# Kernel optimization log

Hardware: AMD Instinct MI355X
Metric: run time of the kernel (lower is better)

Reference implementation:

```python
import jax, jax.numpy as jnp
import numpy as np
from jax import lax

B, T, N, E, M = 2, 24, 1500, 2000, 4000
DIM, NLY, K = 64, 2, 3
H = DIM + DIM // 2  # 96: GAT input dim after concat with NodeEdge output


def setup_inputs():
    ks = iter(jax.random.split(jax.random.key(0), 100))
    def rn(shape, scale=1.0):
        return jax.random.normal(next(ks), shape, dtype=jnp.float32) * scale
    d = {}
    d["x_in"] = rn((B, T, N, 4)); d["e_in"] = rn((B, T, E, 3))
    d["b_in"] = rn((B, T, N, 4)); d["a_in"] = rn((B, T, E, 3))
    def lin(name, din, dout):
        d[name + "_W"] = rn((din, dout), 1.0 / float(np.sqrt(din)))
        d[name + "_b"] = jnp.zeros((dout,), jnp.float32)
    lin("enc0", 4, DIM); lin("enc1", 3, DIM)
    lin("enc2", 4, DIM // 2); lin("enc3", 3, DIM // 2)
    d["inci"] = jax.random.uniform(next(ks), (N, E), dtype=jnp.float32)
    for p in ("s1", "s2"):
        for g in ("gx", "ge"):
            d[p + "_" + g + "_W"] = rn((NLY, H, DIM), 0.1)
            d[p + "_" + g + "_as"] = rn((NLY, DIM), 0.1)
            d[p + "_" + g + "_ad"] = rn((NLY, DIM), 0.1)
            d[p + "_" + g + "_b"] = jnp.zeros((NLY, DIM), jnp.float32)
        d[p + "_ne_W"] = rn((NLY, DIM, DIM // 2), 0.125)
        d[p + "_ne_b"] = jnp.zeros((NLY, DIM // 2), jnp.float32)
        d[p + "_ne_w"] = rn((NLY, N, E), 0.02)
        d[p + "_ne_p"] = jnp.zeros((NLY, N, E), jnp.float32)
        d[p + "_en_W"] = rn((NLY, DIM, DIM // 2), 0.125)
        d[p + "_en_b"] = jnp.zeros((NLY, DIM // 2), jnp.float32)
        d[p + "_en_w"] = rn((NLY, E, N), 0.02)
        d[p + "_en_p"] = jnp.zeros((NLY, E, N), jnp.float32)
        d[p + "_tp_W"] = rn((NLY, DIM, DIM, K), 0.07)
        d[p + "_tp_b"] = jnp.zeros((NLY, DIM), jnp.float32)
    lin("conc", H, DIM); lin("res", DIM, DIM); lin("out", DIM, 1)
    d["edge_ind"] = jax.random.randint(next(ks), (2, E), 0, N)
    d["node_ind"] = jax.random.randint(next(ks), (2, M), 0, E)
    return d


def gat(x, src, dst, n, W, a_s, a_d, bias):
    # PyG GATConv (heads=1, concat=True, neg_slope=0.2); self-loops already in src/dst.
    # x: [B,T,n,din] -> G=B*T independent graphs (the batched edge_index replication
    # of BatchGATConv is exactly equivalent to vmapping over graph replicas).
    g = x.reshape(B * T, n, x.shape[-1])
    z = g @ W                                    # [G,n,DIM]
    es = jnp.einsum('gnd,d->gn', z, a_s)
    ed = jnp.einsum('gnd,d->gn', z, a_d)
    alpha = jax.nn.leaky_relu(es[:, src] + ed[:, dst], 0.2)   # [G,Etot]
    def one(a, zz):
        m = jax.ops.segment_max(a, dst, num_segments=n)
        ex = jnp.exp(a - m[dst])
        s = jax.ops.segment_sum(ex, dst, num_segments=n)
        w = ex / s[dst]
        return jax.ops.segment_sum(w[:, None] * zz[src], dst, num_segments=n)
    out = jax.vmap(one)(alpha, z) + bias
    return out.reshape(B, T, n, DIM)


def node_edge(inp, W, b, w, p, A):
    # NodeEdge: relu(Linear(dim->dim//2)) then incidence-masked matmul
    xe = jax.nn.relu(inp @ W + b)                # [B,T,*,DIM//2]
    return jnp.einsum('ne,btef->btnf', w * A + p, xe)


def causal_conv(h, W, b, dil):
    # h: [M,C,T]; left-pad (K-1)*dil -> causal dilated Conv1d
    pad = (K - 1) * dil
    out = lax.conv_general_dilated(h, W, (1,), [(pad, 0)], rhs_dilation=(dil,),
                                   dimension_numbers=('NCH', 'OIH', 'NCH'))
    return out + b[None, :, None]


def stblock(x, e, src_n, dst_n, src_e, dst_e, inc, P):
    (gxW, gxas, gxad, gxb, geW, geas, gead, geb,
     neW, neb, new, nep, enW, enb, enw, enp, tpW, tpb) = P
    incT = inc.T
    for l in range(NLY):
        xe = node_edge(e, neW[l], neb[l], new[l], nep[l], inc)
        x = jax.nn.relu(gat(jnp.concatenate([x, xe], -1), src_n, dst_n, N,
                            gxW[l], gxas[l], gxad[l], gxb[l]))
        ex = node_edge(x, enW[l], enb[l], enw[l], enp[l], incT)
        e = jax.nn.relu(gat(jnp.concatenate([e, ex], -1), src_e, dst_e, E,
                            geW[l], geas[l], gead[l], geb[l]))
    xt = x.transpose(0, 2, 3, 1).reshape(B * N, DIM, T)   # 'b t n d -> (b n) d t'
    et = e.transpose(0, 2, 3, 1).reshape(B * E, DIM, T)
    h = jnp.concatenate([xt, et], axis=0)
    for l in range(NLY):
        h = jax.nn.relu(causal_conv(h, tpW[l], tpb[l], 2 ** l))
    x = h[:B * N].reshape(B, N, DIM, T).transpose(0, 3, 1, 2)
    e = h[B * N:].reshape(B, E, DIM, T).transpose(0, 3, 1, 2)
    return x, e


def _forward(x_in, e_in, b_in, a_in, enc0_W, enc0_b, enc1_W, enc1_b, enc2_W, enc2_b,
             enc3_W, enc3_b, inci,
             s1_gx_W, s1_gx_as, s1_gx_ad, s1_gx_b, s1_ge_W, s1_ge_as, s1_ge_ad, s1_ge_b,
             s1_ne_W, s1_ne_b, s1_ne_w, s1_ne_p, s1_en_W, s1_en_b, s1_en_w, s1_en_p,
             s1_tp_W, s1_tp_b,
             s2_gx_W, s2_gx_as, s2_gx_ad, s2_gx_b, s2_ge_W, s2_ge_as, s2_ge_ad, s2_ge_b,
             s2_ne_W, s2_ne_b, s2_ne_w, s2_ne_p, s2_en_W, s2_en_b, s2_en_w, s2_en_p,
             s2_tp_W, s2_tp_b,
             conc_W, conc_b, res_W, res_b, out_W, out_b, edge_ind, node_ind):
    # add self-loops once (GATConv add_self_loops=True)
    src_n = jnp.concatenate([edge_ind[0], jnp.arange(N)])
    dst_n = jnp.concatenate([edge_ind[1], jnp.arange(N)])
    src_e = jnp.concatenate([node_ind[0], jnp.arange(E)])
    dst_e = jnp.concatenate([node_ind[1], jnp.arange(E)])
    inc = jnp.abs(inci)
    x = x_in @ enc0_W + enc0_b
    e = e_in @ enc1_W + enc1_b
    bb = jax.nn.relu(b_in @ enc2_W + enc2_b)
    aa = jax.nn.relu(a_in @ enc3_W + enc3_b)
    res_x = jnp.broadcast_to(x[:, -1:], (B, T, N, DIM))   # pre-relu last step, tiled
    res_e = jnp.broadcast_to(e[:, -1:], (B, T, E, DIM))
    x = jax.nn.relu(x); e = jax.nn.relu(e)
    P1 = (s1_gx_W, s1_gx_as, s1_gx_ad, s1_gx_b, s1_ge_W, s1_ge_as, s1_ge_ad, s1_ge_b,
          s1_ne_W, s1_ne_b, s1_ne_w, s1_ne_p, s1_en_W, s1_en_b, s1_en_w, s1_en_p,
          s1_tp_W, s1_tp_b)
    P2 = (s2_gx_W, s2_gx_as, s2_gx_ad, s2_gx_b, s2_ge_W, s2_ge_as, s2_ge_ad, s2_ge_b,
          s2_ne_W, s2_ne_b, s2_ne_w, s2_ne_p, s2_en_W, s2_en_b, s2_en_w, s2_en_p,
          s2_tp_W, s2_tp_b)
    x, e = stblock(x, e, src_n, dst_n, src_e, dst_e, inc, P1)
    # concs is [Linear]*2 in torch -> shared weights for both branches
    x = jax.nn.relu(jnp.concatenate([x, bb], -1) @ conc_W + conc_b)
    e = jax.nn.relu(jnp.concatenate([e, aa], -1) @ conc_W + conc_b)
    x, e = stblock(x, e, src_n, dst_n, src_e, dst_e, inc, P2)
    x = jax.nn.relu(jnp.cumsum(x @ res_W + res_b, axis=1) + res_x)
    e = jax.nn.relu(jnp.cumsum(e @ res_W + res_b, axis=1) + res_e)
    out = jnp.clip((x @ out_W + out_b) / 6.0 + 0.5, 0.0, 1.0)   # F.hardsigmoid
    eo = jnp.tanh(e @ out_W + out_b)
    return out, eo


def reference(x_in, e_in, b_in, a_in, enc0_W, enc0_b, enc1_W, enc1_b, enc2_W, enc2_b,
              enc3_W, enc3_b, inci,
              s1_gx_W, s1_gx_as, s1_gx_ad, s1_gx_b, s1_ge_W, s1_ge_as, s1_ge_ad, s1_ge_b,
              s1_ne_W, s1_ne_b, s1_ne_w, s1_ne_p, s1_en_W, s1_en_b, s1_en_w, s1_en_p,
              s1_tp_W, s1_tp_b,
              s2_gx_W, s2_gx_as, s2_gx_ad, s2_gx_b, s2_ge_W, s2_ge_as, s2_ge_ad, s2_ge_b,
              s2_ne_W, s2_ne_b, s2_ne_w, s2_ne_p, s2_en_W, s2_en_b, s2_en_w, s2_en_p,
              s2_tp_W, s2_tp_b,
              conc_W, conc_b, res_W, res_b, out_W, out_b, edge_ind, node_ind):
    return _forward(x_in, e_in, b_in, a_in, enc0_W, enc0_b, enc1_W, enc1_b, enc2_W,
                    enc2_b, enc3_W, enc3_b, inci,
                    s1_gx_W, s1_gx_as, s1_gx_ad, s1_gx_b, s1_ge_W, s1_ge_as, s1_ge_ad,
                    s1_ge_b, s1_ne_W, s1_ne_b, s1_ne_w, s1_ne_p, s1_en_W, s1_en_b,
                    s1_en_w, s1_en_p, s1_tp_W, s1_tp_b,
                    s2_gx_W, s2_gx_as, s2_gx_ad, s2_gx_b, s2_ge_W, s2_ge_as, s2_ge_ad,
                    s2_ge_b, s2_ne_W, s2_ne_b, s2_ne_w, s2_ne_p, s2_en_W, s2_en_b,
                    s2_en_w, s2_en_p, s2_tp_W, s2_tp_b,
                    conc_W, conc_b, res_W, res_b, out_W, out_b, edge_ind, node_ind)
```

## Files before the change

### kernel.cpp

```cpp
#include <hip/hip_runtime.h>
#include <hip/hip_bf16.h>
#include <cfloat>
#include <math.h>

typedef __hip_bfloat16 bf16;
typedef __attribute__((ext_vector_type(8))) short short8v;
typedef __attribute__((ext_vector_type(4))) float f32x4;

constexpr int B_ = 2, T_ = 24, N_ = 1500, E_ = 2000, M_ = 4000, G_ = 48;
constexpr int KPN = 2048;
constexpr int KPE = 1536;

__device__ __forceinline__ float b2f(bf16 v) { return __bfloat162float(v); }
__device__ __forceinline__ bf16 f2b(float v) { return __float2bfloat16(v); }
static inline int ceilDiv(int a, int b) { return (a + b - 1) / b; }

__global__ __launch_bounds__(256) void k_sentinel(float* __restrict__ out, int n, float val) {
  int i = blockIdx.x * 256 + threadIdx.x;
  if (i < n) out[i] = val;
}

__device__ __forceinline__ void wprep_body(int i, const float* g0, const float* e0, const float* g1,
                                           const float* e1, const float* cw, const float* rw,
                                           const float* t0, const float* t1, bf16* out) {
  if (i >= 108544) return;
  float v;
  if (i < 49152) {
    int which = i / 12288, r = i % 12288;
    const float* W = which == 0 ? g0 : which == 1 ? e0 : which == 2 ? g1 : e1;
    int l = r / 6144, j = r % 6144;
    int n = j / 96, k = j % 96;
    v = W[l * 6144 + k * 64 + n];
  } else if (i < 55296) {
    int j = i - 49152, n = j / 96, k = j % 96;
    v = cw[k * 64 + n];
  } else if (i < 59392) {
    int j = i - 55296, n = j / 64, k = j % 64;
    v = rw[k * 64 + n];
  } else {
    int r = i - 59392;
    int which = r / 24576;
    const float* W = which ? t1 : t0;
    int rr = r % 24576;
    int l = rr / 12288, j = rr % 12288;
    int ii = j & 63, o = (j >> 6) & 63, k = j >> 12;
    v = W[l * 12288 + o * 192 + ii * 3 + k];
  }
  out[i] = f2b(v);
}

__device__ __forceinline__ void enc_body(int idx, int din, const float* in, const float* W,
                                         const float* bias, bf16* out, float* last, int nodes) {
  if (idx >= G_ * nodes * 64) return;
  int d = idx & 63;
  int row = idx >> 6;
  int node = row % nodes;
  int g = row / nodes;
  const float* ir = in + (size_t)row * din;
  float acc = bias[d];
  for (int i = 0; i < din; i++) acc += ir[i] * W[i * 64 + d];
  if (g % T_ == T_ - 1) last[((size_t)(g / T_) * nodes + node) * 64 + d] = acc;
  out[idx] = f2b(fmaxf(acc, 0.f));
}

constexpr int NB_W = (108544 + 255) / 256;
constexpr int NB_EX = G_ * N_ * 64 / 256;
constexpr int NB_EE = G_ * E_ * 64 / 256;
__global__ __launch_bounds__(256) void k_begin(const float* __restrict__ g0, const float* __restrict__ e0,
                                               const float* __restrict__ g1, const float* __restrict__ e1,
                                               const float* __restrict__ cw, const float* __restrict__ rw,
                                               const float* __restrict__ t0, const float* __restrict__ t1,
                                               bf16* __restrict__ wAll,
                                               const float* __restrict__ x_in, const float* __restrict__ encxW,
                                               const float* __restrict__ encxB, bf16* __restrict__ xbuf,
                                               float* __restrict__ lastx,
                                               const float* __restrict__ e_in, const float* __restrict__ enceW,
                                               const float* __restrict__ enceB, bf16* __restrict__ ebuf,
                                               float* __restrict__ laste) {
  int bid = blockIdx.x, tid = threadIdx.x;
  if (bid < NB_W) {
    wprep_body(bid * 256 + tid, g0, e0, g1, e1, cw, rw, t0, t1, wAll);
  } else if (bid < NB_W + NB_EX) {
    enc_body((bid - NB_W) * 256 + tid, 4, x_in, encxW, encxB, xbuf, lastx, N_);
  } else {
    enc_body((bid - NB_W - NB_EX) * 256 + tid, 3, e_in, enceW, enceB, ebuf, laste, E_);
  }
}

template <int DIN, int DOUT>
__global__ __launch_bounds__(256) void k_enc2(const float* __restrict__ in, const float* __restrict__ W,
                                              const float* __restrict__ bias, bf16* __restrict__ out,
                                              int nodes) {
  int idx = blockIdx.x * 256 + threadIdx.x;
  if (idx >= G_ * nodes * DOUT) return;
  int d = idx % DOUT;
  int row = idx / DOUT;
  const float* ir = in + (size_t)row * DIN;
  float acc = bias[d];
#pragma unroll
  for (int i = 0; i < DIN; i++) acc += ir[i] * W[i * DOUT + d];
  out[idx] = f2b(fmaxf(acc, 0.f));
}

__device__ __forceinline__ void lin_neT_body(float* sh, int g, int n0, int t, const bf16* act,
                                             const float* W, const float* bias, bf16* outT,
                                             int nodes, int Kp) {
  float* As = sh;
  float* Ws = sh + 4160;
  float* bs = sh + 4160 + 2048;
  for (int i = t; i < 2048; i += 256) Ws[i] = W[i];
  if (t < 32) bs[t] = bias[t];
  {
    int r = t >> 2, ch = t & 3;
    int node = n0 + r;
    short tmp[16];
    if (node < nodes) {
      const bf16* src = act + ((size_t)g * nodes + node) * 64 + ch * 16;
      *reinterpret_cast<uint4*>(tmp) = *reinterpret_cast<const uint4*>(src);
      *reinterpret_cast<uint4*>(tmp + 8) = *reinterpret_cast<const uint4*>(src + 8);
#pragma unroll
      for (int j = 0; j < 16; j++) As[r * 65 + ch * 16 + j] = b2f(*reinterpret_cast<bf16*>(&tmp[j]));
    } else {
#pragma unroll
      for (int j = 0; j < 16; j++) As[r * 65 + ch * 16 + j] = 0.f;
    }
  }
  __syncthreads();
  int nd = t & 63, fq = t >> 6;
  float acc[8];
#pragma unroll
  for (int j = 0; j < 8; j++) acc[j] = bs[fq * 8 + j];
  for (int i = 0; i < 64; i++) {
    float a = As[nd * 65 + i];
#pragma unroll
    for (int j = 0; j < 8; j++) acc[j] += a * Ws[i * 32 + fq * 8 + j];
  }
  bool valid = (n0 + nd) < nodes;
#pragma unroll
  for (int j = 0; j < 8; j++) {
    float v = valid ? fmaxf(acc[j], 0.f) : 0.f;
    outT[(size_t)(g * 32 + fq * 8 + j) * Kp + n0 + nd] = f2b(v);
  }
}

constexpr int NBL_N = (KPN / 64) * G_;
constexpr int NBM_N = (N_ * KPN + 255) / 256;
__global__ __launch_bounds__(256) void k_prepN(const bf16* __restrict__ act, const float* __restrict__ W,
                                               const float* __restrict__ bias, bf16* __restrict__ outT,
                                               const float* __restrict__ w, const float* __restrict__ p,
                                               const float* __restrict__ inci, bf16* __restrict__ mat) {
  __shared__ float sh[4160 + 2048 + 32];
  int bid = blockIdx.x, tid = threadIdx.x;
  if (bid < NBL_N) {
    lin_neT_body(sh, bid / (KPN / 64), (bid % (KPN / 64)) * 64, tid, act, W, bias, outT, E_, KPN);
  } else {
    int i = (bid - NBL_N) * 256 + tid;
    if (i < N_ * KPN) {
      int row = i / KPN, k = i % KPN;
      float v = 0.f;
      if (k < E_) {
        size_t o = (size_t)row * E_ + k;
        v = w[o] * fabsf(inci[o]) + p[o];
      }
      mat[i] = f2b(v);
    }
  }
}

constexpr int NBL_E = (KPE / 64) * G_;
constexpr int NBT_E = 63 * (KPE / 32);
__global__ __launch_bounds__(256) void k_prepE(const bf16* __restrict__ act, const float* __restrict__ W,
                                               const float* __restrict__ bias, bf16* __restrict__ outT,
                                               const float* __restrict__ w, const float* __restrict__ p,
                                               const float* __restrict__ inci, bf16* __restrict__ mat) {
  __shared__ float sh[4160 + 2048 + 32];
  int bid = blockIdx.x, tid = threadIdx.x;
  if (bid < NBL_E) {
    lin_neT_body(sh, bid / (KPE / 64), (bid % (KPE / 64)) * 64, tid, act, W, bias, outT, N_, KPE);
  } else {
    float* tl = sh;
    int mt = bid - NBL_E;
    int e0 = (mt % 63) * 32, n0 = (mt / 63) * 32;
    int tx = tid & 31, ty = tid >> 5;
    for (int r = ty; r < 32; r += 8) {
      int n = n0 + r, e = e0 + tx;
      tl[r * 33 + tx] = (n < N_ && e < E_) ? fabsf(inci[(size_t)n * E_ + e]) : 0.f;
    }
    __syncthreads();
    for (int r = ty; r < 32; r += 8) {
      int e = e0 + r, n = n0 + tx;
      if (e < E_ && n < KPE) {
        size_t o = (size_t)e * N_ + n;
        mat[(size_t)e * KPE + n] = (n < N_) ? f2b(tl[tx * 33 + r] * w[o] + p[o]) : f2b(0.f);
      }
    }
  }
}

__global__ __launch_bounds__(256) void k_mgemm64(const bf16* __restrict__ A0, const bf16* __restrict__ Bt,
                                                 bf16* __restrict__ Cp, int Mm, int Kp, int Nn, int gy) {
  __shared__ __align__(16) short As[4][4][64][8];
  __shared__ __align__(16) short Bs[4][4][128][8];
  int tid = threadIdx.x;
  int nwg = gridDim.x;
  int bid = blockIdx.x;
  int l = (bid & 7) * (nwg >> 3) + (bid >> 3);
  int bm = (l % gy) * 64, bn = (l / gy) * 128;
  int lane = tid & 63, wid = tid >> 6;
  int wr = wid >> 1, wc = wid & 1;
  f32x4 acc[2][4];
#pragma unroll
  for (int i = 0; i < 2; i++)
#pragma unroll
    for (int j = 0; j < 4; j++) acc[i][j] = f32x4{0.f, 0.f, 0.f, 0.f};

  const int sr = tid >> 2;
  const int sc = tid & 3;
  const int br = tid >> 1;
  const int bh = tid & 1;
  const int kb = lane >> 4, lr = lane & 15;
  const int gmA = bm + sr;
  const bool va_ok = (gmA < Mm);
  const bf16* ap = A0 + (size_t)gmA * Kp + sc * 8;
  const bf16* bp = Bt + (size_t)(bn + br) * Kp + bh * 16;
  const uint4 z4 = {0, 0, 0, 0};
  const int P = Kp >> 5;

  uint4 va0 = va_ok ? *reinterpret_cast<const uint4*>(ap) : z4;
  uint4 vb0a = *reinterpret_cast<const uint4*>(bp);
  uint4 vb0b = *reinterpret_cast<const uint4*>(bp + 8);
  uint4 va1 = va_ok ? *reinterpret_cast<const uint4*>(ap + 32) : z4;
  uint4 vb1a = *reinterpret_cast<const uint4*>(bp + 32);
  uint4 vb1b = *reinterpret_cast<const uint4*>(bp + 40);
  *reinterpret_cast<uint4*>(&As[0][sc][sr][0]) = va0;
  *reinterpret_cast<uint4*>(&Bs[0][bh * 2 + 0][br][0]) = vb0a;
  *reinterpret_cast<uint4*>(&Bs[0][bh * 2 + 1][br][0]) = vb0b;
  uint4 va2 = va_ok ? *reinterpret_cast<const uint4*>(ap + 64) : z4;
  uint4 vb2a = *reinterpret_cast<const uint4*>(bp + 64);
  uint4 vb2b = *reinterpret_cast<const uint4*>(bp + 72);
  __syncthreads();

  for (int p = 0; p < P; p += 2) {
    *reinterpret_cast<uint4*>(&As[(p + 1) & 3][sc][sr][0]) = va1;
    *reinterpret_cast<uint4*>(&Bs[(p + 1) & 3][bh * 2 + 0][br][0]) = vb1a;
    *reinterpret_cast<uint4*>(&Bs[(p + 1) & 3][bh * 2 + 1][br][0]) = vb1b;
    if (p + 3 < P) {
      va1 = va_ok ? *reinterpret_cast<const uint4*>(ap + (p + 3) * 32) : z4;
      vb1a = *reinterpret_cast<const uint4*>(bp + (p + 3) * 32);
      vb1b = *reinterpret_cast<const uint4*>(bp + (p + 3) * 32 + 8);
    }
    {
      int bf = p & 3;
      short8v a0 = *reinterpret_cast<const short8v*>(&As[bf][kb][wr * 32 + lr][0]);
      short8v a1 = *reinterpret_cast<const short8v*>(&As[bf][kb][wr * 32 + 16 + lr][0]);
      short8v b[4];
#pragma unroll
      for (int ni = 0; ni < 4; ni++)
        b[ni] = *reinterpret_cast<const short8v*>(&Bs[bf][kb][wc * 64 + ni * 16 + lr][0]);
      __builtin_amdgcn_s_setprio(1);
#pragma unroll
      for (int ni = 0; ni < 4; ni++) {
        acc[0][ni] = __builtin_amdgcn_mfma_f32_16x16x32_bf16(a0, b[ni], acc[0][ni], 0, 0, 0);
        acc[1][ni] = __builtin_amdgcn_mfma_f32_16x16x32_bf16(a1, b[ni], acc[1][ni], 0, 0, 0);
      }
      __builtin_amdgcn_s_setprio(0);
    }
    __syncthreads();
    *reinterpret_cast<uint4*>(&As[(p + 2) & 3][sc][sr][0]) = va2;
    *reinterpret_cast<uint4*>(&Bs[(p + 2) & 3][bh * 2 + 0][br][0]) = vb2a;
    *reinterpret_cast<uint4*>(&Bs[(p + 2) & 3][bh * 2 + 1][br][0]) = vb2b;
    if (p + 4 < P) {
      va2 = va_ok ? *reinterpret_cast<const uint4*>(ap + (p + 4) * 32) : z4;
      vb2a = *reinterpret_cast<const uint4*>(bp + (p + 4) * 32);
      vb2b = *reinterpret_cast<const uint4*>(bp + (p + 4) * 32 + 8);
    }
    {
      int bf = (p + 1) & 3;
      short8v a0 = *reinterpret_cast<const short8v*>(&As[bf][kb][wr * 32 + lr][0]);
      short8v a1 = *reinterpret_cast<const short8v*>(&As[bf][kb][wr * 32 + 16 + lr][0]);
      short8v b[4];
#pragma unroll
      for (int ni = 0; ni < 4; ni++)
        b[ni] = *reinterpret_cast<const short8v*>(&Bs[bf][kb][wc * 64 + ni * 16 + lr][0]);
      __builtin_amdgcn_s_setprio(1);
#pragma unroll
      for (int ni = 0; ni < 4; ni++) {
        acc[0][ni] = __builtin_amdgcn_mfma_f32_16x16x32_bf16(a0, b[ni], acc[0][ni], 0, 0, 0);
        acc[1][ni] = __builtin_amdgcn_mfma_f32_16x16x32_bf16(a1, b[ni], acc[1][ni], 0, 0, 0);
      }
      __builtin_amdgcn_s_setprio(0);
    }
    __syncthreads();
  }
#pragma unroll
  for (int mi = 0; mi < 2; mi++) {
    int r0 = bm + wr * 32 + mi * 16 + (lane >> 4) * 4;
#pragma unroll
    for (int ni = 0; ni < 4; ni++) {
      int col = bn + wc * 64 + ni * 16 + lr;
#pragma unroll
      for (int i = 0; i < 4; i++) {
        int r = r0 + i;
        if (r < Mm) Cp[(size_t)r * Nn + col] = f2b(acc[mi][ni][i]);
      }
    }
  }
}

template <int AMODE, int KOCT, bool CF32b, bool ESED>
__global__ __launch_bounds__(256) void k_mgemm96(const bf16* __restrict__ A0, const bf16* __restrict__ A1,
                                                 const bf16* __restrict__ Bt, void* __restrict__ Cp,
                                                 int Mm, int nodes,
                                                 const float* __restrict__ bias, int relu,
                                                 const float* __restrict__ asv, const float* __restrict__ adv,
                                                 float* __restrict__ esOut, float* __restrict__ edOut) {
  constexpr int KP = KOCT * 8;
  __shared__ __align__(16) short As[KOCT][128][8];
  __shared__ __align__(16) short Bs[KOCT][64][8];
  __shared__ float smr[2][128][2];
  int tid = threadIdx.x;
  int bm = blockIdx.y * 128;
  int lane = tid & 63, wid = tid >> 6;
  int wr = wid >> 1, wc = wid & 1;
  const int kb = lane >> 4, lr = lane & 15;
  const uint4 z4 = {0, 0, 0, 0};

  {
    int ar = tid >> 1, ah = tid & 1;
    int gm = bm + ar;
    bool ok = (gm < Mm);
    int gdiv = 0, gmod = 0;
    if (AMODE == 1 && ok) { gdiv = gm / nodes; gmod = gm % nodes; }
#pragma unroll
    for (int c = 0; c < KOCT / 4; c++) {
      int ks = c * 32 + ah * 16;
      uint4 va0 = z4, va1 = z4;
      if (ok) {
        const bf16* src;
        if (AMODE == 0) src = A0 + (size_t)gm * KP + ks;
        else if (ks < 64) src = A0 + (size_t)gm * 64 + ks;
        else if (AMODE == 1) src = A1 + ((size_t)gmod * G_ + gdiv) * 32 + (ks - 64);
        else src = A1 + (size_t)gm * 32 + (ks - 64);
        const uint4* p = reinterpret_cast<const uint4*>(src);
        va0 = p[0];
        va1 = p[1];
      }
      *reinterpret_cast<uint4*>(&As[c * 4 + ah * 2 + 0][ar][0]) = va0;
      *reinterpret_cast<uint4*>(&As[c * 4 + ah * 2 + 1][ar][0]) = va1;
    }
  }
  {
    int br = tid >> 2, bk = tid & 3;
#pragma unroll
    for (int c = 0; c < KOCT / 4; c++) {
      int o = c * 4 + bk;
      uint4 vb = *reinterpret_cast<const uint4*>(Bt + (size_t)br * KP + o * 8);
      *reinterpret_cast<uint4*>(&Bs[o][br][0]) = vb;
    }
  }
  __syncthreads();

  f32x4 acc[4][2];
#pragma unroll
  for (int i = 0; i < 4; i++)
#pragma unroll
    for (int j = 0; j < 2; j++) acc[i][j] = f32x4{0.f, 0.f, 0.f, 0.f};

#pragma unroll
  for (int c = 0; c < KOCT / 4; c++) {
    short8v a[4], b[2];
#pragma unroll
    for (int mi = 0; mi < 4; mi++)
      a[mi] = *reinterpret_cast<const short8v*>(&As[c * 4 + kb][wr * 64 + mi * 16 + lr][0]);
#pragma unroll
    for (int ni = 0; ni < 2; ni++)
      b[ni] = *reinterpret_cast<const short8v*>(&Bs[c * 4 + kb][wc * 32 + ni * 16 + lr][0]);
    __builtin_amdgcn_s_setprio(1);
#pragma unroll
    for (int mi = 0; mi < 4; mi++)
#pragma unroll
      for (int ni = 0; ni < 2; ni++)
        acc[mi][ni] = __builtin_amdgcn_mfma_f32_16x16x32_bf16(a[mi], b[ni], acc[mi][ni], 0, 0, 0);
    __builtin_amdgcn_s_setprio(0);
  }

#pragma unroll
  for (int mi = 0; mi < 4; mi++) {
    int r0 = bm + wr * 64 + mi * 16 + (lane >> 4) * 4;
#pragma unroll
    for (int ni = 0; ni < 2; ni++) {
      int col = wc * 32 + ni * 16 + lr;
      float bv = bias ? bias[col] : 0.f;
#pragma unroll
      for (int i = 0; i < 4; i++) {
        int r = r0 + i;
        if (r < Mm) {
          float v = acc[mi][ni][i] + bv;
          if (relu) v = fmaxf(v, 0.f);
          if (CF32b) ((float*)Cp)[(size_t)r * 64 + col] = v;
          else ((bf16*)Cp)[(size_t)r * 64 + col] = f2b(v);
        }
      }
    }
  }
  if (ESED) {
    float asc0 = asv[wc * 32 + lr];
    float asc1 = asv[wc * 32 + 16 + lr];
    float adc0 = adv[wc * 32 + lr];
    float adc1 = adv[wc * 32 + 16 + lr];
#pragma unroll
    for (int mi = 0; mi < 4; mi++) {
#pragma unroll
      for (int i = 0; i < 4; i++) {
        float pe = acc[mi][0][i] * asc0 + acc[mi][1][i] * asc1;
        float pd = acc[mi][0][i] * adc0 + acc[mi][1][i] * adc1;
#pragma unroll
        for (int o = 8; o; o >>= 1) { pe += __shfl_xor(pe, o); pd += __shfl_xor(pd, o); }
        if (lr == 0) {
          int rl = wr * 64 + mi * 16 + (lane >> 4) * 4 + i;
          smr[wc][rl][0] = pe;
          smr[wc][rl][1] = pd;
        }
      }
    }
    __syncthreads();
    if (tid < 128) {
      int r = bm + tid;
      if (r < Mm) {
        esOut[r] = smr[0][tid][0] + smr[1][tid][0];
        edOut[r] = smr[0][tid][1] + smr[1][tid][1];
      }
    }
  }
}

template <int DIL>
__global__ __launch_bounds__(256) void k_cgemm2(const bf16* __restrict__ Ax, bf16* __restrict__ Cx,
                                                int Mx, int nx, const bf16* __restrict__ Ae,
                                                bf16* __restrict__ Ce, int Me, int ne, int nbx,
                                                const bf16* __restrict__ Wc, const float* __restrict__ bias) {
  __shared__ __align__(16) short As[4][4][128][8];
  int tid = threadIdx.x;
  int bid = blockIdx.x;
  const bf16* A;
  bf16* C;
  int Mm, nodes, bm;
  if (bid < nbx) { A = Ax; C = Cx; Mm = Mx; nodes = nx; bm = bid * 128; }
  else { A = Ae; C = Ce; Mm = Me; nodes = ne; bm = (bid - nbx) * 128; }
  int lane = tid & 63, wid = tid >> 6;
  int wr = wid >> 1, wc = wid & 1;
  const int ar = tid >> 1, ah = tid & 1;
  const int kb = lane >> 4, lr = lane & 15;
  const int gm = bm + ar;
  const int t = (gm / nodes) % T_;
  const uint4 z4 = {0, 0, 0, 0};

  short8v bfr[3][2][2];
#pragma unroll
  for (int tap = 0; tap < 3; tap++)
#pragma unroll
    for (int kc = 0; kc < 2; kc++)
#pragma unroll
      for (int ni = 0; ni < 2; ni++) {
        int col = wc * 32 + ni * 16 + lr;
        bfr[tap][kc][ni] = *reinterpret_cast<const short8v*>(Wc + tap * 4096 + (size_t)col * 64 + kc * 32 + kb * 8);
      }

  f32x4 acc[4][2];
#pragma unroll
  for (int i = 0; i < 4; i++)
#pragma unroll
    for (int j = 0; j < 2; j++) acc[i][j] = f32x4{0.f, 0.f, 0.f, 0.f};

#define CG_LDA(p, vx, vy)                                                          \
  {                                                                                \
    const int sh_ = (((p) >> 1) - 2) * DIL;                                        \
    if ((gm < Mm) && (t + sh_ >= 0)) {                                             \
      const uint4* pp = reinterpret_cast<const uint4*>(                            \
          A + ((size_t)gm + (size_t)sh_ * nodes) * 64 + ((p) & 1) * 32 + ah * 16); \
      vx = pp[0];                                                                  \
      vy = pp[1];                                                                  \
    } else {                                                                       \
      vx = z4;                                                                     \
      vy = z4;                                                                     \
    }                                                                              \
  }
#define CG_WR(buf, vx, vy)                                     \
  *reinterpret_cast<uint4*>(&As[buf][ah * 2 + 0][ar][0]) = vx; \
  *reinterpret_cast<uint4*>(&As[buf][ah * 2 + 1][ar][0]) = vy;
#define CG_MFMA(q)                                                                                         \
  {                                                                                                        \
    short8v a0_ = *reinterpret_cast<const short8v*>(&As[(q) & 3][kb][wr * 64 + 0 + lr][0]);                \
    short8v a1_ = *reinterpret_cast<const short8v*>(&As[(q) & 3][kb][wr * 64 + 16 + lr][0]);               \
    short8v a2_ = *reinterpret_cast<const short8v*>(&As[(q) & 3][kb][wr * 64 + 32 + lr][0]);               \
    short8v a3_ = *reinterpret_cast<const short8v*>(&As[(q) & 3][kb][wr * 64 + 48 + lr][0]);               \
    __builtin_amdgcn_s_setprio(1);                                                                         \
    acc[0][0] = __builtin_amdgcn_mfma_f32_16x16x32_bf16(a0_, bfr[(q) >> 1][(q) & 1][0], acc[0][0], 0, 0, 0); \
    acc[0][1] = __builtin_amdgcn_mfma_f32_16x16x32_bf16(a0_, bfr[(q) >> 1][(q) & 1][1], acc[0][1], 0, 0, 0); \
    acc[1][0] = __builtin_amdgcn_mfma_f32_16x16x32_bf16(a1_, bfr[(q) >> 1][(q) & 1][0], acc[1][0], 0, 0, 0); \
    acc[1][1] = __builtin_amdgcn_mfma_f32_16x16x32_bf16(a1_, bfr[(q) >> 1][(q) & 1][1], acc[1][1], 0, 0, 0); \
    acc[2][0] = __builtin_amdgcn_mfma_f32_16x16x32_bf16(a2_, bfr[(q) >> 1][(q) & 1][0], acc[2][0], 0, 0, 0); \
    acc[2][1] = __builtin_amdgcn_mfma_f32_16x16x32_bf16(a2_, bfr[(q) >> 1][(q) & 1][1], acc[2][1], 0, 0, 0); \
    acc[3][0] = __builtin_amdgcn_mfma_f32_16x16x32_bf16(a3_, bfr[(q) >> 1][(q) & 1][0], acc[3][0], 0, 0, 0); \
    acc[3][1] = __builtin_amdgcn_mfma_f32_16x16x32_bf16(a3_, bfr[(q) >> 1][(q) & 1][1], acc[3][1], 0, 0, 0); \
    __builtin_amdgcn_s_setprio(0);                                                                         \
  }
#define CG_BODY(p, lastPair)                  \
  CG_WR(((p) + 1) & 3, r1x, r1y);             \
  if (!(lastPair)) CG_LDA((p) + 3, r1x, r1y); \
  CG_MFMA(p);                                 \
  __syncthreads();                            \
  CG_WR(((p) + 2) & 3, r2x, r2y);             \
  if (!(lastPair)) CG_LDA((p) + 4, r2x, r2y); \
  CG_MFMA((p) + 1);                           \
  __syncthreads();

  uint4 p0x, p0y, r1x, r1y, r2x, r2y;
  CG_LDA(0, p0x, p0y);
  CG_LDA(1, r1x, r1y);
  CG_WR(0, p0x, p0y);
  CG_LDA(2, r2x, r2y);
  __syncthreads();

  CG_BODY(0, false)
  CG_BODY(2, false)
  CG_BODY(4, true)

#undef CG_LDA
#undef CG_WR
#undef CG_MFMA
#undef CG_BODY

#pragma unroll
  for (int mi = 0; mi < 4; mi++) {
    int r0 = bm + wr * 64 + mi * 16 + (lane >> 4) * 4;
#pragma unroll
    for (int ni = 0; ni < 2; ni++) {
      int col = wc * 32 + ni * 16 + lr;
      float bv = bias[col];
#pragma unroll
      for (int i = 0; i < 4; i++) {
        int r = r0 + i;
        if (r < Mm) C[(size_t)r * 64 + col] = f2b(fmaxf(acc[mi][ni][i] + bv, 0.f));
      }
    }
  }
}

__global__ __launch_bounds__(256) void k_gat_w(const float* __restrict__ es, const float* __restrict__ edv,
                                               const int* __restrict__ off, const int* __restrict__ adj,
                                               float* __restrict__ wgt, int nodes, int tot) {
  int idx = blockIdx.x * 256 + threadIdx.x;
  if (idx >= G_ * nodes) return;
  int g = idx / nodes, node = idx % nodes;
  int s0 = off[node], s1 = off[node + 1];
  const float* esg = es + (size_t)g * nodes;
  float edval = edv[(size_t)g * nodes + node];
  float m = -FLT_MAX;
  for (int s = s0; s < s1; s++) {
    float a = esg[adj[s]] + edval;
    a = (a >= 0.f) ? a : 0.2f * a;
    m = fmaxf(m, a);
  }
  float den = 0.f;
  float* wg = wgt + (size_t)g * tot;
  for (int s = s0; s < s1; s++) {
    float a = esg[adj[s]] + edval;
    a = (a >= 0.f) ? a : 0.2f * a;
    float ex = expf(a - m);
    den += ex;
    wg[s] = ex;
  }
  float inv = (s1 > s0) ? 1.f / den : 0.f;
  for (int s = s0; s < s1; s++) wg[s] *= inv;
}

__global__ __launch_bounds__(256) void k_gat_aggr3(const bf16* __restrict__ z, const float* __restrict__ wgt,
                                                   const int* __restrict__ off, const int* __restrict__ adj,
                                                   const float* __restrict__ bias, bf16* __restrict__ out,
                                                   int nodes, int tot) {
  int idx = blockIdx.x * 256 + threadIdx.x;
  if (idx >= G_ * nodes * 16) return;
  int c = idx & 15;
  int rest = idx >> 4;
  int node = rest % nodes;
  int g = rest / nodes;
  int s0 = off[node], s1 = off[node + 1];
  const bf16* zg = z + (size_t)g * nodes * 64 + c * 4;
  const float* wg = wgt + (size_t)g * tot;
  float n0 = 0.f, n1 = 0.f, n2 = 0.f, n3 = 0.f;
  for (int s = s0; s < s1; s++) {
    int src = adj[s];
    float w = wg[s];
    bf16 v[4];
    *reinterpret_cast<uint2*>(v) = *reinterpret_cast<const uint2*>(zg + (size_t)src * 64);
    n0 += w * b2f(v[0]);
    n1 += w * b2f(v[1]);
    n2 += w * b2f(v[2]);
    n3 += w * b2f(v[3]);
  }
  bf16 ov[4];
  ov[0] = f2b(fmaxf(n0 + bias[c * 4 + 0], 0.f));
  ov[1] = f2b(fmaxf(n1 + bias[c * 4 + 1], 0.f));
  ov[2] = f2b(fmaxf(n2 + bias[c * 4 + 2], 0.f));
  ov[3] = f2b(fmaxf(n3 + bias[c * 4 + 3], 0.f));
  *reinterpret_cast<uint2*>(out + (size_t)rest * 64 + c * 4) = *reinterpret_cast<uint2*>(ov);
}

__global__ __launch_bounds__(1024) void k_csr(const int* __restrict__ indN, const int* __restrict__ indE,
                                              int* __restrict__ offN, int* __restrict__ adjN,
                                              int* __restrict__ offE, int* __restrict__ adjE) {
  __shared__ int cnt[2048];
  __shared__ int a[1024];
  const int* ind;
  int ner, nn;
  int *off, *adj;
  if (blockIdx.x == 0) { ind = indN; ner = E_; nn = N_; off = offN; adj = adjN; }
  else { ind = indE; ner = M_; nn = E_; off = offE; adj = adjE; }
  int tot = ner + nn;
  int t = threadIdx.x;
  for (int i = t; i < nn; i += 1024) cnt[i] = 0;
  __syncthreads();
  for (int i = t; i < tot; i += 1024) {
    int d = (i < ner) ? ind[ner + i] : (i - ner);
    if (d >= 0 && d < nn) atomicAdd(&cnt[d], 1);
  }
  __syncthreads();
  int c0 = (2 * t < nn) ? cnt[2 * t] : 0;
  int c1 = (2 * t + 1 < nn) ? cnt[2 * t + 1] : 0;
  a[t] = c0 + c1;
  __syncthreads();
  for (int d = 1; d < 1024; d <<= 1) {
    int u = (t >= d) ? a[t - d] : 0;
    __syncthreads();
    a[t] += u;
    __syncthreads();
  }
  int excl = (t > 0) ? a[t - 1] : 0;
  if (2 * t < nn) { cnt[2 * t] = excl; off[2 * t] = excl; }
  if (2 * t + 1 < nn) { cnt[2 * t + 1] = excl + c0; off[2 * t + 1] = excl + c0; }
  if (t == 0) off[nn] = a[1023];
  __syncthreads();
  for (int i = t; i < tot; i += 1024) {
    int s, d;
    if (i < ner) { s = ind[i]; d = ind[ner + i]; }
    else { s = d = i - ner; }
    if (d >= 0 && d < nn) {
      int pos = atomicAdd(&cnt[d], 1);
      adj[pos] = s;
    }
  }
}

template <bool XB>
__global__ __launch_bounds__(256) void k_out(const float* __restrict__ yx, const float* __restrict__ last,
                                             const float* __restrict__ oW, const float* __restrict__ ob_,
                                             float* __restrict__ dout, int nodes, int batches) {
  int wid = threadIdx.x >> 6, lane = threadIdx.x & 63;
  int idx = blockIdx.x * 4 + wid;
  if (idx >= batches * nodes) return;
  int b = idx / nodes, node = idx % nodes;
  const float* yb = yx + (size_t)b * T_ * nodes * 64;
  float lw = oW[lane];
  float ob = ob_[0];
  float lv = last[(size_t)idx * 64 + lane];
  float acc = 0.f;
  for (int tt = 0; tt < T_; tt++) {
    acc += yb[((size_t)tt * nodes + node) * 64 + lane];
    float v = fmaxf(acc + lv, 0.f);
    float p = v * lw;
#pragma unroll
    for (int o2 = 32; o2; o2 >>= 1) p += __shfl_down(p, o2);
    if (lane == 0) {
      float o = p + ob;
      if (XB) o = fminf(fmaxf(o / 6.f + 0.5f, 0.f), 1.f);
      else o = tanhf(o);
      dout[(size_t)b * T_ * nodes + (size_t)tt * nodes + node] = o;
    }
  }
}

extern "C" void kernel_launch(void* const* d_in, const int* in_sizes, int n_in,
                              void* d_out, int out_size, void* d_ws, size_t ws_size,
                              hipStream_t stream) {
  float* dout = (float*)d_out;

  if (n_in != 57) {
    k_sentinel<<<ceilDiv(out_size, 256), 256, 0, stream>>>(dout, out_size, 20000.f + 128.f * n_in);
    return;
  }
  static const int expSz[57] = {
      288000, 288000, 288000, 288000,
      256, 64, 192, 64, 128, 32, 96, 32,
      3000000,
      12288, 128, 128, 128, 12288, 128, 128, 128,
      4096, 64, 6000000, 6000000, 4096, 64, 6000000, 6000000,
      24576, 128,
      12288, 128, 128, 128, 12288, 128, 128, 128,
      4096, 64, 6000000, 6000000, 4096, 64, 6000000, 6000000,
      24576, 128,
      6144, 64, 4096, 64, 64, 1, 4000, 8000};
  for (int i = 0; i < 57; i++) {
    if (in_sizes[i] != expSz[i]) {
      k_sentinel<<<ceilDiv(out_size, 256), 256, 0, stream>>>(dout, out_size, 4096.f + 64.f * i);
      return;
    }
  }

  auto ff = [&](int i) { return (const float*)d_in[i]; };
  const float *x_in = ff(0), *e_in = ff(1), *b_in = ff(2), *a_in = ff(3);
  const float *enc0W = ff(4), *enc0b = ff(5), *enc1W = ff(6), *enc1b = ff(7);
  const float *enc2W = ff(8), *enc2b = ff(9), *enc3W = ff(10), *enc3b = ff(11);
  const float* inci = ff(12);
  const float *concW = ff(49), *concb = ff(50), *resW = ff(51), *resb = ff(52);
  const float *outW = ff(53), *outb = ff(54);
  const int* edge_ind = (const int*)d_in[55];
  const int* node_ind = (const int*)d_in[56];

  char* base = (char*)d_ws;
  size_t off = 0;
  auto A = [&](size_t bytes) { void* p = base + off; off = (off + bytes + 255) & ~(size_t)255; return p; };
  char* SCR = (char*)A(21504000);
  bf16* xbuf = (bf16*)A(9216000);
  bf16* ebuf = (bf16*)A(12288000);
  float* lastx = (float*)A(768000);
  float* laste = (float*)A(1024000);
  float* es = (float*)A(384000);
  float* edv = (float*)A(384000);
  float* wgt = (float*)A((size_t)G_ * (M_ + E_) * 4);
  bf16* wAll = (bf16*)A(217088);
  int* offN = (int*)A((N_ + 1) * 4);
  int* offE = (int*)A((E_ + 1) * 4);
  int* adjN = (int*)A((E_ + N_) * 4);
  int* adjE = (int*)A((M_ + E_) * 4);
  size_t required = off;

  if (ws_size < required) {
    k_sentinel<<<ceilDiv(out_size, 256), 256, 0, stream>>>(dout, out_size, 1000.f + (float)(ws_size >> 20));
    return;
  }

  bf16* matb = (bf16*)SCR;
  bf16* tlinT = (bf16*)(SCR + 6553600);
  bf16* tmat = (bf16*)(SCR + 13107200);
  bf16* zbuf = (bf16*)SCR;
  bf16* bscr = (bf16*)SCR;
  bf16* cx1 = (bf16*)SCR;
  bf16* ce1 = (bf16*)(SCR + 9216000);
  float* zres = (float*)SCR;

  const int totN = E_ + N_;
  const int totE = M_ + E_;
  const int nbx = ceilDiv(G_ * N_, 128);
  const int nbe = ceilDiv(G_ * E_, 128);

  k_begin<<<NB_W + NB_EX + NB_EE, 256, 0, stream>>>(
      ff(13), ff(17), ff(31), ff(35), concW, resW, ff(29), ff(47), wAll,
      x_in, enc0W, enc0b, xbuf, lastx, e_in, enc1W, enc1b, ebuf, laste);
  k_csr<<<2, 1024, 0, stream>>>(edge_ind, node_ind, offN, adjN, offE, adjE);

  auto stblock = [&](int sb, int sbi) {
    const float *gxas = ff(sb + 1), *gxad = ff(sb + 2), *gxb = ff(sb + 3);
    const float *geas = ff(sb + 5), *gead = ff(sb + 6), *geb = ff(sb + 7);
    const float *neW = ff(sb + 8), *neb = ff(sb + 9), *nw = ff(sb + 10), *np_ = ff(sb + 11);
    const float *enW = ff(sb + 12), *enb = ff(sb + 13), *ew = ff(sb + 14), *ep = ff(sb + 15);
    const float* tpb = ff(sb + 17);
    for (int l = 0; l < 2; l++) {
      const bf16* gxw_t = wAll + sbi * 24576 + l * 6144;
      const bf16* gew_t = wAll + sbi * 24576 + 12288 + l * 6144;
      k_prepN<<<NBL_N + NBM_N, 256, 0, stream>>>(ebuf, neW + l * 2048, neb + l * 32, tlinT,
                                                 nw + (size_t)l * N_ * E_, np_ + (size_t)l * N_ * E_, inci, matb);
      k_mgemm64<<<dim3(12 * 24), 256, 0, stream>>>(matb, tlinT, tmat, N_, KPN, 1536, 24);
      k_mgemm96<1, 12, false, true><<<dim3(1, nbx), 256, 0, stream>>>(
          xbuf, tmat, gxw_t, zbuf, G_ * N_, N_, nullptr, 0, gxas + l * 64, gxad + l * 64, es, edv);
      k_gat_w<<<ceilDiv(G_ * N_, 256), 256, 0, stream>>>(es, edv, offN, adjN, wgt, N_, totN);
      k_gat_aggr3<<<ceilDiv(G_ * N_ * 16, 256), 256, 0, stream>>>(zbuf, wgt, offN, adjN, gxb + l * 64, xbuf, N_, totN);
      k_prepE<<<NBL_E + NBT_E, 256, 0, stream>>>(xbuf, enW + l * 2048, enb + l * 32, tlinT,
                                                 ew + (size_t)l * E_ * N_, ep + (size_t)l * E_ * N_, inci, matb);
      k_mgemm64<<<dim3(12 * 32), 256, 0, stream>>>(matb, tlinT, tmat, E_, KPE, 1536, 32);
      k_mgemm96<1, 12, false, true><<<dim3(1, nbe), 256, 0, stream>>>(
          ebuf, tmat, gew_t, zbuf, G_ * E_, E_, nullptr, 0, geas + l * 64, gead + l * 64, es, edv);
      k_gat_w<<<ceilDiv(G_ * E_, 256), 256, 0, stream>>>(es, edv, offE, adjE, wgt, E_, totE);
      k_gat_aggr3<<<ceilDiv(G_ * E_ * 16, 256), 256, 0, stream>>>(zbuf, wgt, offE, adjE, geb + l * 64, ebuf, E_, totE);
    }
    const bf16* cw0 = wAll + 59392 + sbi * 24576;
    const bf16* cw1 = cw0 + 12288;
    k_cgemm2<1><<<nbx + nbe, 256, 0, stream>>>(xbuf, cx1, G_ * N_, N_, ebuf, ce1, G_ * E_, E_, nbx, cw0, tpb);
    k_cgemm2<2><<<nbx + nbe, 256, 0, stream>>>(cx1, xbuf, G_ * N_, N_, ce1, ebuf, G_ * E_, E_, nbx, cw1, tpb + 64);
  };

  stblock(13, 0);

  const bf16* concT = wAll + 49152;
  k_enc2<4, 32><<<ceilDiv(G_ * N_ * 32, 256), 256, 0, stream>>>(b_in, enc2W, enc2b, bscr, N_);
  k_mgemm96<2, 12, false, false><<<dim3(1, nbx), 256, 0, stream>>>(
      xbuf, bscr, concT, xbuf, G_ * N_, 0, concb, 1, nullptr, nullptr, nullptr, nullptr);
  k_enc2<3, 32><<<ceilDiv(G_ * E_ * 32, 256), 256, 0, stream>>>(a_in, enc3W, enc3b, bscr, E_);
  k_mgemm96<2, 12, false, false><<<dim3(1, nbe), 256, 0, stream>>>(
      ebuf, bscr, concT, ebuf, G_ * E_, 0, concb, 1, nullptr, nullptr, nullptr, nullptr);

  stblock(31, 1);

  const bf16* resT = wAll + 55296;
  k_mgemm96<0, 8, true, false><<<dim3(1, nbx), 256, 0, stream>>>(
      xbuf, nullptr, resT, zres, G_ * N_, 0, resb, 0, nullptr, nullptr, nullptr, nullptr);
  k_out<true><<<ceilDiv(B_ * N_, 4), 256, 0, stream>>>(zres, lastx, outW, outb, dout, N_, B_);
  for (int b = 0; b < B_; b++) {
    k_mgemm96<0, 8, true, false><<<dim3(1, ceilDiv(T_ * E_, 128)), 256, 0, stream>>>(
        ebuf + (size_t)b * T_ * E_ * 64, nullptr, resT, zres, T_ * E_, 0, resb, 0,
        nullptr, nullptr, nullptr, nullptr);
    k_out<false><<<ceilDiv(E_, 4), 256, 0, stream>>>(
        zres, laste + (size_t)b * E_ * 64, outW, outb, dout + (size_t)(B_ * T_ * N_) + (size_t)b * T_ * E_, E_, 1);
  }
}
```

Measured before the change: 925.2 us.

## Enlarge incidence GEMM tile to 128x128 and fuse GAT softmax into aggregation

The incidence-matrix GEMM now computes 128x128 output tiles per workgroup instead of 64x128, giving each wave 16 MFMAs per k-step and reusing each B fragment across more rows. The grid is halved to match. Separately, the GAT softmax-weight kernel and the aggregation kernel are merged, so each of the 16 channel threads recomputes the attention logits and normalizes at the end. This removes one launch and the write and read of the weight buffer per GAT call, at the cost of redundant exp and logit work and fewer workgroups for the GEMM on a chip with many CUs.

```diff
diff --git a/kernel.cpp b/kernel.cpp
--- a/kernel.cpp
+++ b/kernel.cpp
@@ -199,102 +199,110 @@
 
 __global__ __launch_bounds__(256) void k_mgemm64(const bf16* __restrict__ A0, const bf16* __restrict__ Bt,
                                                  bf16* __restrict__ Cp, int Mm, int Kp, int Nn, int gy) {
-  __shared__ __align__(16) short As[4][4][64][8];
+  __shared__ __align__(16) short As[4][4][128][8];
   __shared__ __align__(16) short Bs[4][4][128][8];
   int tid = threadIdx.x;
   int nwg = gridDim.x;
   int bid = blockIdx.x;
   int l = (bid & 7) * (nwg >> 3) + (bid >> 3);
-  int bm = (l % gy) * 64, bn = (l / gy) * 128;
+  int bm = (l % gy) * 128, bn = (l / gy) * 128;
   int lane = tid & 63, wid = tid >> 6;
   int wr = wid >> 1, wc = wid & 1;
-  f32x4 acc[2][4];
-#pragma unroll
-  for (int i = 0; i < 2; i++)
+  f32x4 acc[4][4];
+#pragma unroll
+  for (int i = 0; i < 4; i++)
 #pragma unroll
     for (int j = 0; j < 4; j++) acc[i][j] = f32x4{0.f, 0.f, 0.f, 0.f};
 
-  const int sr = tid >> 2;
-  const int sc = tid & 3;
-  const int br = tid >> 1;
-  const int bh = tid & 1;
+  const int sr = tid >> 1;
+  const int ah = tid & 1;
   const int kb = lane >> 4, lr = lane & 15;
   const int gmA = bm + sr;
   const bool va_ok = (gmA < Mm);
-  const bf16* ap = A0 + (size_t)gmA * Kp + sc * 8;
-  const bf16* bp = Bt + (size_t)(bn + br) * Kp + bh * 16;
+  const bf16* ap = A0 + (size_t)gmA * Kp + ah * 16;
+  const bf16* bp = Bt + (size_t)(bn + sr) * Kp + ah * 16;
   const uint4 z4 = {0, 0, 0, 0};
   const int P = Kp >> 5;
 
-  uint4 va0 = va_ok ? *reinterpret_cast<const uint4*>(ap) : z4;
+  uint4 va0a = va_ok ? *reinterpret_cast<const uint4*>(ap) : z4;
+  uint4 va0b = va_ok ? *reinterpret_cast<const uint4*>(ap + 8) : z4;
   uint4 vb0a = *reinterpret_cast<const uint4*>(bp);
   uint4 vb0b = *reinterpret_cast<const uint4*>(bp + 8);
-  uint4 va1 = va_ok ? *reinterpret_cast<const uint4*>(ap + 32) : z4;
+  *reinterpret_cast<uint4*>(&As[0][ah * 2 + 0][sr][0]) = va0a;
+  *reinterpret_cast<uint4*>(&As[0][ah * 2 + 1][sr][0]) = va0b;
+  *reinterpret_cast<uint4*>(&Bs[0][ah * 2 + 0][sr][0]) = vb0a;
+  *reinterpret_cast<uint4*>(&Bs[0][ah * 2 + 1][sr][0]) = vb0b;
+  uint4 va1a = va_ok ? *reinterpret_cast<const uint4*>(ap + 32) : z4;
+  uint4 va1b = va_ok ? *reinterpret_cast<const uint4*>(ap + 40) : z4;
   uint4 vb1a = *reinterpret_cast<const uint4*>(bp + 32);
   uint4 vb1b = *reinterpret_cast<const uint4*>(bp + 40);
-  *reinterpret_cast<uint4*>(&As[0][sc][sr][0]) = va0;
-  *reinterpret_cast<uint4*>(&Bs[0][bh * 2 + 0][br][0]) = vb0a;
-  *reinterpret_cast<uint4*>(&Bs[0][bh * 2 + 1][br][0]) = vb0b;
-  uint4 va2 = va_ok ? *reinterpret_cast<const uint4*>(ap + 64) : z4;
+  uint4 va2a = va_ok ? *reinterpret_cast<const uint4*>(ap + 64) : z4;
+  uint4 va2b = va_ok ? *reinterpret_cast<const uint4*>(ap + 72) : z4;
   uint4 vb2a = *reinterpret_cast<const uint4*>(bp + 64);
   uint4 vb2b = *reinterpret_cast<const uint4*>(bp + 72);
   __syncthreads();
 
   for (int p = 0; p < P; p += 2) {
-    *reinterpret_cast<uint4*>(&As[(p + 1) & 3][sc][sr][0]) = va1;
-    *reinterpret_cast<uint4*>(&Bs[(p + 1) & 3][bh * 2 + 0][br][0]) = vb1a;
-    *reinterpret_cast<uint4*>(&Bs[(p + 1) & 3][bh * 2 + 1][br][0]) = vb1b;
+    *reinterpret_cast<uint4*>(&As[(p + 1) & 3][ah * 2 + 0][sr][0]) = va1a;
+    *reinterpret_cast<uint4*>(&As[(p + 1) & 3][ah * 2 + 1][sr][0]) = va1b;
+    *reinterpret_cast<uint4*>(&Bs[(p + 1) & 3][ah * 2 + 0][sr][0]) = vb1a;
+    *reinterpret_cast<uint4*>(&Bs[(p + 1) & 3][ah * 2 + 1][sr][0]) = vb1b;
     if (p + 3 < P) {
-      va1 = va_ok ? *reinterpret_cast<const uint4*>(ap + (p + 3) * 32) : z4;
+      va1a = va_ok ? *reinterpret_cast<const uint4*>(ap + (p + 3) * 32) : z4;
+      va1b = va_ok ? *reinterpret_cast<const uint4*>(ap + (p + 3) * 32 + 8) : z4;
       vb1a = *reinterpret_cast<const uint4*>(bp + (p + 3) * 32);
       vb1b = *reinterpret_cast<const uint4*>(bp + (p + 3) * 32 + 8);
     }
     {
       int bf = p & 3;
-      short8v a0 = *reinterpret_cast<const short8v*>(&As[bf][kb][wr * 32 + lr][0]);
-      short8v a1 = *reinterpret_cast<const short8v*>(&As[bf][kb][wr * 32 + 16 + lr][0]);
-      short8v b[4];
+      short8v a[4], b[4];
+#pragma unroll
+      for (int mi = 0; mi < 4; mi++)
+        a[mi] = *reinterpret_cast<const short8v*>(&As[bf][kb][wr * 64 + mi * 16 + lr][0]);
 #pragma unroll
       for (int ni = 0; ni < 4; ni++)
         b[ni] = *reinterpret_cast<const short8v*>(&Bs[bf][kb][wc * 64 + ni * 16 + lr][0]);
       __builtin_amdgcn_s_setprio(1);
 #pragma unroll
-      for (int ni = 0; ni < 4; ni++) {
-        acc[0][ni] = __builtin_amdgcn_mfma_f32_16x16x32_bf16(a0, b[ni], acc[0][ni], 0, 0, 0);
-        acc[1][ni] = __builtin_amdgcn_mfma_f32_16x16x32_bf16(a1, b[ni], acc[1][ni], 0, 0, 0);
-      }
+      for (int mi = 0; mi < 4; mi++)
+#pragma unroll
+        for (int ni = 0; ni < 4; ni++)
+          acc[mi][ni] = __builtin_amdgcn_mfma_f32_16x16x32_bf16(a[mi], b[ni], acc[mi][ni], 0, 0, 0);
       __builtin_amdgcn_s_setprio(0);
     }
     __syncthreads();
-    *reinterpret_cast<uint4*>(&As[(p + 2) & 3][sc][sr][0]) = va2;
-    *reinterpret_cast<uint4*>(&Bs[(p + 2) & 3][bh * 2 + 0][br][0]) = vb2a;
-    *reinterpret_cast<uint4*>(&Bs[(p + 2) & 3][bh * 2 + 1][br][0]) = vb2b;
+    *reinterpret_cast<uint4*>(&As[(p + 2) & 3][ah * 2 + 0][sr][0]) = va2a;
+    *reinterpret_cast<uint4*>(&As[(p + 2) & 3][ah * 2 + 1][sr][0]) = va2b;
+    *reinterpret_cast<uint4*>(&Bs[(p + 2) & 3][ah * 2 + 0][sr][0]) = vb2a;
+    *reinterpret_cast<uint4*>(&Bs[(p + 2) & 3][ah * 2 + 1][sr][0]) = vb2b;
     if (p + 4 < P) {
-      va2 = va_ok ? *reinterpret_cast<const uint4*>(ap + (p + 4) * 32) : z4;
+      va2a = va_ok ? *reinterpret_cast<const uint4*>(ap + (p + 4) * 32) : z4;
+      va2b = va_ok ? *reinterpret_cast<const uint4*>(ap + (p + 4) * 32 + 8) : z4;
       vb2a = *reinterpret_cast<const uint4*>(bp + (p + 4) * 32);
       vb2b = *reinterpret_cast<const uint4*>(bp + (p + 4) * 32 + 8);
     }
     {
       int bf = (p + 1) & 3;
-      short8v a0 = *reinterpret_cast<const short8v*>(&As[bf][kb][wr * 32 + lr][0]);
-      short8v a1 = *reinterpret_cast<const short8v*>(&As[bf][kb][wr * 32 + 16 + lr][0]);
-      short8v b[4];
+      short8v a[4], b[4];
+#pragma unroll
+      for (int mi = 0; mi < 4; mi++)
+        a[mi] = *reinterpret_cast<const short8v*>(&As[bf][kb][wr * 64 + mi * 16 + lr][0]);
 #pragma unroll
       for (int ni = 0; ni < 4; ni++)
         b[ni] = *reinterpret_cast<const short8v*>(&Bs[bf][kb][wc * 64 + ni * 16 + lr][0]);
       __builtin_amdgcn_s_setprio(1);
 #pragma unroll
-      for (int ni = 0; ni < 4; ni++) {
-        acc[0][ni] = __builtin_amdgcn_mfma_f32_16x16x32_bf16(a0, b[ni], acc[0][ni], 0, 0, 0);
-        acc[1][ni] = __builtin_amdgcn_mfma_f32_16x16x32_bf16(a1, b[ni], acc[1][ni], 0, 0, 0);
-      }
+      for (int mi = 0; mi < 4; mi++)
+#pragma unroll
+        for (int ni = 0; ni < 4; ni++)
+          acc[mi][ni] = __builtin_amdgcn_mfma_f32_16x16x32_bf16(a[mi], b[ni], acc[mi][ni], 0, 0, 0);
       __builtin_amdgcn_s_setprio(0);
     }
     __syncthreads();
   }
 #pragma unroll
-  for (int mi = 0; mi < 2; mi++) {
-    int r0 = bm + wr * 32 + mi * 16 + (lane >> 4) * 4;
+  for (int mi = 0; mi < 4; mi++) {
+    int r0 = bm + wr * 64 + mi * 16 + (lane >> 4) * 4;
 #pragma unroll
     for (int ni = 0; ni < 4; ni++) {
       int col = bn + wc * 64 + ni * 16 + lr;
@@ -547,38 +555,10 @@
   }
 }
 
-__global__ __launch_bounds__(256) void k_gat_w(const float* __restrict__ es, const float* __restrict__ edv,
-                                               const int* __restrict__ off, const int* __restrict__ adj,
-                                               float* __restrict__ wgt, int nodes, int tot) {
-  int idx = blockIdx.x * 256 + threadIdx.x;
-  if (idx >= G_ * nodes) return;
-  int g = idx / nodes, node = idx % nodes;
-  int s0 = off[node], s1 = off[node + 1];
-  const float* esg = es + (size_t)g * nodes;
-  float edval = edv[(size_t)g * nodes + node];
-  float m = -FLT_MAX;
-  for (int s = s0; s < s1; s++) {
-    float a = esg[adj[s]] + edval;
-    a = (a >= 0.f) ? a : 0.2f * a;
-    m = fmaxf(m, a);
-  }
-  float den = 0.f;
-  float* wg = wgt + (size_t)g * tot;
-  for (int s = s0; s < s1; s++) {
-    float a = esg[adj[s]] + edval;
-    a = (a >= 0.f) ? a : 0.2f * a;
-    float ex = expf(a - m);
-    den += ex;
-    wg[s] = ex;
-  }
-  float inv = (s1 > s0) ? 1.f / den : 0.f;
-  for (int s = s0; s < s1; s++) wg[s] *= inv;
-}
-
-__global__ __launch_bounds__(256) void k_gat_aggr3(const bf16* __restrict__ z, const float* __restrict__ wgt,
-                                                   const int* __restrict__ off, const int* __restrict__ adj,
-                                                   const float* __restrict__ bias, bf16* __restrict__ out,
-                                                   int nodes, int tot) {
+__global__ __launch_bounds__(256) void k_gat3(const bf16* __restrict__ z, const float* __restrict__ es,
+                                              const float* __restrict__ edv, const int* __restrict__ off,
+                                              const int* __restrict__ adj, const float* __restrict__ bias,
+                                              bf16* __restrict__ out, int nodes) {
   int idx = blockIdx.x * 256 + threadIdx.x;
   if (idx >= G_ * nodes * 16) return;
   int c = idx & 15;
@@ -586,24 +566,35 @@
   int node = rest % nodes;
   int g = rest / nodes;
   int s0 = off[node], s1 = off[node + 1];
+  const float* esg = es + (size_t)g * nodes;
+  float edval = edv[(size_t)g * nodes + node];
   const bf16* zg = z + (size_t)g * nodes * 64 + c * 4;
-  const float* wg = wgt + (size_t)g * tot;
-  float n0 = 0.f, n1 = 0.f, n2 = 0.f, n3 = 0.f;
+  float m = -FLT_MAX;
+  for (int s = s0; s < s1; s++) {
+    float a = esg[adj[s]] + edval;
+    a = (a >= 0.f) ? a : 0.2f * a;
+    m = fmaxf(m, a);
+  }
+  float den = 0.f, n0 = 0.f, n1 = 0.f, n2 = 0.f, n3 = 0.f;
   for (int s = s0; s < s1; s++) {
     int src = adj[s];
-    float w = wg[s];
+    float a = esg[src] + edval;
+    a = (a >= 0.f) ? a : 0.2f * a;
+    float ex = expf(a - m);
+    den += ex;
     bf16 v[4];
     *reinterpret_cast<uint2*>(v) = *reinterpret_cast<const uint2*>(zg + (size_t)src * 64);
-    n0 += w * b2f(v[0]);
-    n1 += w * b2f(v[1]);
-    n2 += w * b2f(v[2]);
-    n3 += w * b2f(v[3]);
-  }
+    n0 += ex * b2f(v[0]);
+    n1 += ex * b2f(v[1]);
+    n2 += ex * b2f(v[2]);
+    n3 += ex * b2f(v[3]);
+  }
+  float inv = (s1 > s0) ? 1.f / den : 0.f;
   bf16 ov[4];
-  ov[0] = f2b(fmaxf(n0 + bias[c * 4 + 0], 0.f));
-  ov[1] = f2b(fmaxf(n1 + bias[c * 4 + 1], 0.f));
-  ov[2] = f2b(fmaxf(n2 + bias[c * 4 + 2], 0.f));
-  ov[3] = f2b(fmaxf(n3 + bias[c * 4 + 3], 0.f));
+  ov[0] = f2b(fmaxf(n0 * inv + bias[c * 4 + 0], 0.f));
+  ov[1] = f2b(fmaxf(n1 * inv + bias[c * 4 + 1], 0.f));
+  ov[2] = f2b(fmaxf(n2 * inv + bias[c * 4 + 2], 0.f));
+  ov[3] = f2b(fmaxf(n3 * inv + bias[c * 4 + 3], 0.f));
   *reinterpret_cast<uint2*>(out + (size_t)rest * 64 + c * 4) = *reinterpret_cast<uint2*>(ov);
 }
 
@@ -727,7 +718,6 @@
   float* laste = (float*)A(1024000);
   float* es = (float*)A(384000);
   float* edv = (float*)A(384000);
-  float* wgt = (float*)A((size_t)G_ * (M_ + E_) * 4);
   bf16* wAll = (bf16*)A(217088);
   int* offN = (int*)A((N_ + 1) * 4);
   int* offE = (int*)A((E_ + 1) * 4);
@@ -749,8 +739,6 @@
   bf16* ce1 = (bf16*)(SCR + 9216000);
   float* zres = (float*)SCR;
 
-  const int totN = E_ + N_;
-  const int totE = M_ + E_;
   const int nbx = ceilDiv(G_ * N_, 128);
   const int nbe = ceilDiv(G_ * E_, 128);
 
@@ -770,18 +758,16 @@
       const bf16* gew_t = wAll + sbi * 24576 + 12288 + l * 6144;
       k_prepN<<<NBL_N + NBM_N, 256, 0, stream>>>(ebuf, neW + l * 2048, neb + l * 32, tlinT,
                                                  nw + (size_t)l * N_ * E_, np_ + (size_t)l * N_ * E_, inci, matb);
-      k_mgemm64<<<dim3(12 * 24), 256, 0, stream>>>(matb, tlinT, tmat, N_, KPN, 1536, 24);
+      k_mgemm64<<<dim3(12 * 12), 256, 0, stream>>>(matb, tlinT, tmat, N_, KPN, 1536, 12);
       k_mgemm96<1, 12, false, true><<<dim3(1, nbx), 256, 0, stream>>>(
           xbuf, tmat, gxw_t, zbuf, G_ * N_, N_, nullptr, 0, gxas + l * 64, gxad + l * 64, es, edv);
-      k_gat_w<<<ceilDiv(G_ * N_, 256), 256, 0, stream>>>(es, edv, offN, adjN, wgt, N_, totN);
-      k_gat_aggr3<<<ceilDiv(G_ * N_ * 16, 256), 256, 0, stream>>>(zbuf, wgt, offN, adjN, gxb + l * 64, xbuf, N_, totN);
+      k_gat3<<<ceilDiv(G_ * N_ * 16, 256), 256, 0, stream>>>(zbuf, es, edv, offN, adjN, gxb + l * 64, xbuf, N_);
       k_prepE<<<NBL_E + NBT_E, 256, 0, stream>>>(xbuf, enW + l * 2048, enb + l * 32, tlinT,
                                                  ew + (size_t)l * E_ * N_, ep + (size_t)l * E_ * N_, inci, matb);
-      k_mgemm64<<<dim3(12 * 32), 256, 0, stream>>>(matb, tlinT, tmat, E_, KPE, 1536, 32);
+      k_mgemm64<<<dim3(16 * 12), 256, 0, stream>>>(matb, tlinT, tmat, E_, KPE, 1536, 16);
       k_mgemm96<1, 12, false, true><<<dim3(1, nbe), 256, 0, stream>>>(
           ebuf, tmat, gew_t, zbuf, G_ * E_, E_, nullptr, 0, geas + l * 64, gead + l * 64, es, edv);
-      k_gat_w<<<ceilDiv(G_ * E_, 256), 256, 0, stream>>>(es, edv, offE, adjE, wgt, E_, totE);
-      k_gat_aggr3<<<ceilDiv(G_ * E_ * 16, 256), 256, 0, stream>>>(zbuf, wgt, offE, adjE, geb + l * 64, ebuf, E_, totE);
+      k_gat3<<<ceilDiv(G_ * E_ * 16, 256), 256, 0, stream>>>(zbuf, es, edv, offE, adjE, geb + l * 64, ebuf, E_);
     }
     const bf16* cw0 = wAll + 59392 + sbi * 24576;
     const bf16* cw1 = cw0 + 12288;
```

Result: no change. 941.8 us (+1.8%).
